# Optimization experiments

Measured on AMD Instinct MI355X. Metric: run time of the kernel, lower is better.

## Reference

```python
import jax, jax.numpy as jnp
import numpy as np
import math

H = 2048
NH = 16
HD = H // NH  # 128
EPS_LN = 1e-5
RES_SCALE_MAX = 0.3

def _nan_clean(x, lim=10000.0):
    return jnp.nan_to_num(x, nan=0.0, posinf=lim, neginf=-lim)

def setup_inputs() -> dict:
    key = jax.random.key(0)
    ks = jax.random.split(key, 12)
    B, S, T = 4, 2048, 256
    std = 1.0 / math.sqrt(H)
    return {
        "hidden_states": jax.random.normal(ks[0], (B, S, H), jnp.float32),
        "audio_tokens": jax.random.normal(ks[1], (B, T, H), jnp.float32),
        "attention_mask": jax.random.randint(ks[2], (B, T), 0, 2, jnp.int32),
        "Wq": jax.random.normal(ks[3], (H, H), jnp.float32) * std,
        "bq": jnp.zeros((H,), jnp.float32),
        "Wk": jax.random.normal(ks[4], (H, H), jnp.float32) * std,
        "bk": jnp.zeros((H,), jnp.float32),
        "Wv": jax.random.normal(ks[5], (H, H), jnp.float32) * std,
        "bv": jnp.zeros((H,), jnp.float32),
        "Wo": jax.random.normal(ks[6], (H, H), jnp.float32) * std,
        "bo": jnp.zeros((H,), jnp.float32),
        "ln_gamma": jnp.ones((H,), jnp.float32),
        "ln_beta": jnp.zeros((H,), jnp.float32),
        "residual_scale": jnp.float32(0.05),
    }

def reference(hidden_states, audio_tokens, attention_mask,
              Wq, bq, Wk, bk, Wv, bv, Wo, bo, ln_gamma, ln_beta, residual_scale):
    B, S, _ = hidden_states.shape
    T = audio_tokens.shape[1]
    hs = _nan_clean(hidden_states).astype(jnp.float32)
    at = _nan_clean(audio_tokens).astype(jnp.float32)
    # Q/K/V projections -> (B, heads, len, head_dim)
    def proj(x, W, b, L):
        y = x @ W.T + b
        return y.reshape(B, L, NH, HD).transpose(0, 2, 1, 3)
    q = _nan_clean(proj(hs, Wq, bq, S))
    k = _nan_clean(proj(at, Wk, bk, T))
    v = _nan_clean(proj(at, Wv, bv, T))
    scale = max(math.sqrt(HD), 1e-8)
    scores = jnp.einsum('bhsd,bhtd->bhst', q, k) / scale
    scores = jnp.clip(scores, -50.0, 50.0)
    scores = jnp.nan_to_num(scores, nan=0.0, posinf=50.0, neginf=-50.0)
    # mask: int 0/1 -> attend where > 0.5, broadcast (B,1,1,T)
    attend = (attention_mask.astype(jnp.float32) > 0.5)[:, None, None, :]
    scores = jnp.where(attend, scores, -10000.0)
    scores = jnp.clip(scores, -50.0, 50.0)
    probs = jax.nn.softmax(scores, axis=-1)
    probs = jnp.nan_to_num(probs, nan=0.0, posinf=1.0, neginf=0.0)
    probs = probs / (probs.sum(axis=-1, keepdims=True) + 1e-8)
    # dropout: eval mode -> identity
    ctx = jnp.einsum('bhst,bhtd->bhsd', probs, v)
    ctx = ctx.transpose(0, 2, 1, 3).reshape(B, S, H)
    delta = _nan_clean(ctx @ Wo.T + bo)
    rs = jnp.clip(residual_scale, 0.0, RES_SCALE_MAX)
    delta = rs * delta
    # LayerNorm (biased variance, like torch)
    mu = delta.mean(axis=-1, keepdims=True)
    var = jnp.mean((delta - mu) ** 2, axis=-1, keepdims=True)
    delta = (delta - mu) / jnp.sqrt(var + EPS_LN) * ln_gamma + ln_beta
    return delta
```

## Files before the change

kernel.cpp:

```cpp
#include <hip/hip_runtime.h>
#include <stdint.h>

typedef unsigned short u16;
typedef __attribute__((ext_vector_type(8))) __bf16 bf16x8;
typedef __attribute__((ext_vector_type(4))) float f32x4;

#define AS1 __attribute__((address_space(1)))
#define AS3 __attribute__((address_space(3)))

constexpr int HB = 4;
constexpr int SS = 2048;
constexpr int TT = 256;
constexpr int HH = 2048;
constexpr int NHEAD = 16;
constexpr int HD = 128;

__device__ __forceinline__ u16 f2b(float f) {
  union { float f; uint32_t u; } c; c.f = f;
  return (u16)((c.u + 0x7FFFu + ((c.u >> 16) & 1u)) >> 16);
}

__device__ __forceinline__ float b2f(uint32_t lo16) {
  union { uint32_t u; float f; } c; c.u = lo16 << 16;
  return c.f;
}

__global__ __launch_bounds__(256)
void cast_kernel(const float* __restrict__ in, u16* __restrict__ out, int n4) {
  int i = blockIdx.x * 256 + threadIdx.x;
  if (i >= n4) return;
  const float4 v = *(const float4*)(in + (size_t)i * 4);
  uint2 pk;
  pk.x = (uint32_t)f2b(v.x) | ((uint32_t)f2b(v.y) << 16);
  pk.y = (uint32_t)f2b(v.z) | ((uint32_t)f2b(v.w) << 16);
  *(uint2*)(out + (size_t)i * 4) = pk;
}

__global__ __launch_bounds__(256)
void cast_w_kernel(const float* __restrict__ w0, const float* __restrict__ w1,
                   const float* __restrict__ w2, const float* __restrict__ w3,
                   u16* __restrict__ o0, u16* __restrict__ o1,
                   u16* __restrict__ o2, u16* __restrict__ o3) {
  const float* src; u16* dst;
  switch (blockIdx.y) {
    case 0: src = w0; dst = o0; break;
    case 1: src = w1; dst = o1; break;
    case 2: src = w2; dst = o2; break;
    default: src = w3; dst = o3; break;
  }
  const int i = blockIdx.x * 256 + threadIdx.x;
  const float4 v = *(const float4*)(src + (size_t)i * 4);
  uint2 pk;
  pk.x = (uint32_t)f2b(v.x) | ((uint32_t)f2b(v.y) << 16);
  pk.y = (uint32_t)f2b(v.z) | ((uint32_t)f2b(v.w) << 16);
  *(uint2*)(dst + (size_t)i * 4) = pk;
}

template<int MODE>
__global__ __launch_bounds__(512, 2)
void gemm8(const u16* __restrict__ A, const u16* __restrict__ Bw,
           const float* __restrict__ bias, const float* __restrict__ rsp,
           void* __restrict__ outp) {
  constexpr int KD = 2048, NT = 64;
  constexpr int BUF = 16384;
  __shared__ u16 lds[3 * BUF];
  const int tid = threadIdx.x;
  const int wv = tid >> 6, ln = tid & 63;
  const int lq = ln >> 4, lr = ln & 15;
  const int wm = wv >> 2, wn = wv & 3;

  const int linb = blockIdx.y * 8 + blockIdx.x;
  const int ns = (linb & 7) * 32 + (linb >> 3);
  const int m0 = (ns >> 3) * 256;
  const int n0 = (ns & 7) * 256;

  int gOff[2];
#pragma unroll
  for (int c = 0; c < 2; ++c) {
    const int g = c * 512 + tid, sr = g >> 3, s = g & 7, l = s ^ (sr & 7);
    gOff[c] = (2 * sr + (l >> 2)) * KD + (l & 3) * 8;
  }
  const u16* Abase = A + (size_t)m0 * KD;
  const u16* Bbase = Bw + (size_t)n0 * KD;

  int aoff[8], boff[4];
#pragma unroll
  for (int m = 0; m < 8; ++m) {
    const int R = wm * 128 + m * 16 + lr, sr = R >> 1;
    aoff[m] = sr * 64 + ((((R & 1) << 2) + lq) ^ (sr & 7)) * 8;
  }
#pragma unroll
  for (int j = 0; j < 4; ++j) {
    const int R = wn * 64 + j * 16 + lr, sr = R >> 1;
    boff[j] = 8192 + sr * 64 + ((((R & 1) << 2) + lq) ^ (sr & 7)) * 8;
  }

#define STAGE_A(c, k0, buf)                                                      \
  __builtin_amdgcn_global_load_lds((AS1 const void*)(Abase + (k0) + gOff[c]),    \
      (AS3 void*)(lds + (buf) * BUF + ((c) * 512 + wv * 64) * 8), 16, 0, 0)
#define STAGE_B(c, k0, buf)                                                      \
  __builtin_amdgcn_global_load_lds((AS1 const void*)(Bbase + (k0) + gOff[c]),    \
      (AS3 void*)(lds + (buf) * BUF + 8192 + ((c) * 512 + wv * 64) * 8), 16, 0, 0)

  f32x4 acc[8][4];
#pragma unroll
  for (int i = 0; i < 8; ++i)
#pragma unroll
    for (int j = 0; j < 4; ++j) acc[i][j] = (f32x4){0.f, 0.f, 0.f, 0.f};

  STAGE_A(0, 0, 0); STAGE_A(1, 0, 0); STAGE_B(0, 0, 0); STAGE_B(1, 0, 0);
  STAGE_A(0, 32, 1); STAGE_A(1, 32, 1); STAGE_B(0, 32, 1); STAGE_B(1, 32, 1);
  asm volatile("s_waitcnt vmcnt(4)" ::: "memory");
  __builtin_amdgcn_s_barrier();

  int cur = 0;
  for (int t = 0; t < NT; ++t) {
    const u16* bb = lds + cur * BUF;
    const int stg = (cur >= 1) ? cur - 1 : 2;
    const int k2 = (t + 2) * 32;
    const bool doStage = (t + 2) < NT;
    bf16x8 af[4], bf[4];

#pragma unroll
    for (int j = 0; j < 4; ++j) bf[j] = *(const bf16x8*)(bb + boff[j]);
#pragma unroll
    for (int m = 0; m < 4; ++m) af[m] = *(const bf16x8*)(bb + aoff[m]);
    if (doStage) { STAGE_A(0, k2, stg); STAGE_A(1, k2, stg); }
    __builtin_amdgcn_s_barrier();
    asm volatile("s_waitcnt lgkmcnt(0)" ::: "memory");
    __builtin_amdgcn_sched_barrier(0);
    __builtin_amdgcn_s_setprio(1);
#pragma unroll
    for (int m = 0; m < 4; ++m)
#pragma unroll
      for (int j = 0; j < 4; ++j)
        acc[m][j] = __builtin_amdgcn_mfma_f32_16x16x32_bf16(af[m], bf[j], acc[m][j], 0, 0, 0);
    __builtin_amdgcn_s_setprio(0);
    __builtin_amdgcn_s_barrier();

#pragma unroll
    for (int m = 0; m < 4; ++m) af[m] = *(const bf16x8*)(bb + aoff[4 + m]);
    if (doStage) { STAGE_B(0, k2, stg); STAGE_B(1, k2, stg); }
    if (t < NT - 2)      asm volatile("s_waitcnt vmcnt(4)" ::: "memory");
    else if (t == NT - 2) asm volatile("s_waitcnt vmcnt(0)" ::: "memory");
    __builtin_amdgcn_s_barrier();
    asm volatile("s_waitcnt lgkmcnt(0)" ::: "memory");
    __builtin_amdgcn_sched_barrier(0);
    __builtin_amdgcn_s_setprio(1);
#pragma unroll
    for (int m = 0; m < 4; ++m)
#pragma unroll
      for (int j = 0; j < 4; ++j)
        acc[4 + m][j] = __builtin_amdgcn_mfma_f32_16x16x32_bf16(af[m], bf[j], acc[4 + m][j], 0, 0, 0);
    __builtin_amdgcn_s_setprio(0);
    __builtin_amdgcn_s_barrier();

    cur = (cur + 1 == 3) ? 0 : cur + 1;
  }
#undef STAGE_A
#undef STAGE_B

  float bj[4];
#pragma unroll
  for (int j = 0; j < 4; ++j) bj[j] = bias[n0 + wn * 64 + j * 16 + lr];
  float rsv = 0.f;
  if constexpr (MODE == 2 || MODE == 3) rsv = fminf(fmaxf(rsp[0], 0.0f), 0.3f);

#pragma unroll
  for (int i = 0; i < 8; ++i)
#pragma unroll
    for (int j = 0; j < 4; ++j)
#pragma unroll
      for (int r = 0; r < 4; ++r) {
        const int row = m0 + wm * 128 + i * 16 + lq * 4 + r;
        const int col = n0 + wn * 64 + j * 16 + lr;
        const float v = acc[i][j][r] + bj[j];
        if constexpr (MODE == 0) {
          ((u16*)outp)[(size_t)row * 2048 + col] = f2b(v);
        } else if constexpr (MODE == 2) {
          ((float*)outp)[(size_t)row * 2048 + col] = v * rsv;
        } else {
          ((u16*)outp)[(size_t)row * 2048 + col] = f2b(v * rsv);
        }
      }
}

__global__ __launch_bounds__(256, 2)
void gemm_kv(const u16* __restrict__ A, const u16* __restrict__ Wk,
             const u16* __restrict__ Wv, const float* __restrict__ bkp,
             const float* __restrict__ bvp, u16* __restrict__ Ko,
             u16* __restrict__ Vto) {
  constexpr int KD = 2048;
  __shared__ u16 sA[128 * 32];
  __shared__ u16 sB[128 * 32];
  const bool isV = blockIdx.z != 0;
  const u16* Bw = isV ? Wv : Wk;
  const float* bias = isV ? bvp : bkp;
  const int tid = threadIdx.x;
  const int wave = tid >> 6, lane = tid & 63;
  const int lq = lane >> 4, lr = lane & 15;
  const int wr = wave >> 1, wc = wave & 1;
  const int m0 = blockIdx.y * 128, n0 = blockIdx.x * 128;

  f32x4 acc[4][4];
#pragma unroll
  for (int i = 0; i < 4; ++i)
#pragma unroll
    for (int j = 0; j < 4; ++j) acc[i][j] = (f32x4){0.f, 0.f, 0.f, 0.f};

  for (int k0 = 0; k0 < KD; k0 += 32) {
#pragma unroll
    for (int it = 0; it < 2; ++it) {
      const int c = wave * 128 + it * 64 + lane;
      const int row = c >> 2, cc = c & 3;
      const u16* ga = A + (size_t)(m0 + row) * KD + (k0 + cc * 8);
      const u16* gb = Bw + (size_t)(n0 + row) * KD + (k0 + cc * 8);
      u16* la = sA + (size_t)(wave * 128 + it * 64) * 8;
      u16* lb = sB + (size_t)(wave * 128 + it * 64) * 8;
      __builtin_amdgcn_global_load_lds((AS1 const void*)ga, (AS3 void*)la, 16, 0, 0);
      __builtin_amdgcn_global_load_lds((AS1 const void*)gb, (AS3 void*)lb, 16, 0, 0);
    }
    asm volatile("s_waitcnt vmcnt(0)" ::: "memory");
    __syncthreads();

    bf16x8 af[4], bfr[4];
#pragma unroll
    for (int i = 0; i < 4; ++i)
      af[i] = *(const bf16x8*)(sA + (size_t)(wr * 64 + i * 16 + lr) * 32 + lq * 8);
#pragma unroll
    for (int j = 0; j < 4; ++j)
      bfr[j] = *(const bf16x8*)(sB + (size_t)(wc * 64 + j * 16 + lr) * 32 + lq * 8);
#pragma unroll
    for (int i = 0; i < 4; ++i)
#pragma unroll
      for (int j = 0; j < 4; ++j)
        acc[i][j] = __builtin_amdgcn_mfma_f32_16x16x32_bf16(af[i], bfr[j], acc[i][j], 0, 0, 0);
    __syncthreads();
  }

  float bj[4];
#pragma unroll
  for (int j = 0; j < 4; ++j) bj[j] = bias[n0 + wc * 64 + j * 16 + lr];

#pragma unroll
  for (int i = 0; i < 4; ++i)
#pragma unroll
    for (int j = 0; j < 4; ++j)
#pragma unroll
      for (int r = 0; r < 4; ++r) {
        const int row = m0 + wr * 64 + i * 16 + lq * 4 + r;
        const int col = n0 + wc * 64 + j * 16 + lr;
        const float v = acc[i][j][r] + bj[j];
        if (!isV) {
          Ko[(size_t)row * 2048 + col] = f2b(v);
        } else {
          Vto[(size_t)(row >> 8) * (2048 * 256) + (size_t)col * 256 + (row & 255)] = f2b(v);
        }
      }
}

__global__ __launch_bounds__(512, 2)
void attn_kernel(const u16* __restrict__ Q, const u16* __restrict__ Kb,
                 const u16* __restrict__ Vt, const int* __restrict__ mask,
                 u16* __restrict__ ctx) {
  __shared__ u16 sQ[128 * 128];
  __shared__ u16 sK[2][64 * 128];
  __shared__ u16 sVt[2][128 * 64];
  __shared__ u16 sP[8 * 16 * 72];

  const int tid = threadIdx.x;
  const int wv = tid >> 6, ln = tid & 63;
  const int lq = ln >> 4, lr = ln & 15;
  const int h = blockIdx.y, b = blockIdx.z;
  const int s0blk = blockIdx.x * 128;
  u16* sPw = sP + wv * (16 * 72);

  {
    const size_t qg = ((size_t)b * SS + s0blk) * HH + (size_t)h * HD;
#pragma unroll
    for (int it = 0; it < 4; ++it) {
      const int ub = it * 512 + wv * 64;
      const int u = ub + ln;
      const int row = u >> 4, slot = u & 15, src = slot ^ (row & 15);
      __builtin_amdgcn_global_load_lds((AS1 const void*)(Q + qg + (size_t)row * HH + src * 8),
                                       (AS3 void*)(sQ + (size_t)ub * 8), 16, 0, 0);
    }
  }
#define STAGE_KV(c)                                                                      \
  {                                                                                      \
    const int buf_ = (c) & 1;                                                            \
    _Pragma("unroll")                                                                    \
    for (int it = 0; it < 2; ++it) {                                                     \
      const int ub = it * 512 + wv * 64;                                                 \
      const int u = ub + ln;                                                             \
      const int row = u >> 4, slot = u & 15, src = slot ^ (row & 15);                    \
      const u16* g = Kb + ((size_t)b * TT + (c) * 64 + row) * HH + h * HD + src * 8;     \
      __builtin_amdgcn_global_load_lds((AS1 const void*)g,                               \
          (AS3 void*)(sK[buf_] + (size_t)ub * 8), 16, 0, 0);                             \
    }                                                                                    \
    _Pragma("unroll")                                                                    \
    for (int it = 0; it < 2; ++it) {                                                     \
      const int ub = it * 512 + wv * 64;                                                 \
      const int u = ub + ln;                                                             \
      const int row = u >> 3, slot = u & 7, src = slot ^ (row & 7);                      \
      const u16* g = Vt + ((size_t)b * HH + h * HD + row) * TT + (c) * 64 + src * 8;     \
      __builtin_amdgcn_global_load_lds((AS1 const void*)g,                               \
          (AS3 void*)(sVt[buf_] + (size_t)ub * 8), 16, 0, 0);                            \
    }                                                                                    \
  }
  STAGE_KV(0);
  STAGE_KV(1);

  const float scale = 0.08838834764831845f;
  float m[4] = {-INFINITY, -INFINITY, -INFINITY, -INFINITY};
  float l[4] = {0.f, 0.f, 0.f, 0.f};
  f32x4 o[8];
#pragma unroll
  for (int d0 = 0; d0 < 8; ++d0) o[d0] = (f32x4){0.f, 0.f, 0.f, 0.f};

  const int qrow = wv * 16 + lr;
  const int shsrc = ((lr >> 2) << 4) + lr;

  for (int c = 0; c < 4; ++c) {
    const int buf = c & 1;
    if (c < 3) asm volatile("s_waitcnt vmcnt(4)" ::: "memory");
    else       asm volatile("s_waitcnt vmcnt(0)" ::: "memory");
    __syncthreads();

    bf16x8 qf[4];
#pragma unroll
    for (int kd = 0; kd < 4; ++kd)
      qf[kd] = *(const bf16x8*)(sQ + (size_t)qrow * 128 + (size_t)((kd * 4 + lq) ^ lr) * 8);

    f32x4 sc[4];
#pragma unroll
    for (int tt = 0; tt < 4; ++tt) {
      f32x4 a = (f32x4){0.f, 0.f, 0.f, 0.f};
#pragma unroll
      for (int kd = 0; kd < 4; ++kd) {
        bf16x8 kf = *(const bf16x8*)(sK[buf] + (size_t)(tt * 16 + lr) * 128 + (size_t)((kd * 4 + lq) ^ lr) * 8);
        a = __builtin_amdgcn_mfma_f32_16x16x32_bf16(qf[kd], kf, a, 0, 0, 0);
      }
      sc[tt] = a;
    }

    float lm[4] = {-1e30f, -1e30f, -1e30f, -1e30f};
#pragma unroll
    for (int tt = 0; tt < 4; ++tt) {
      const int att = mask[b * TT + c * 64 + tt * 16 + lr];
#pragma unroll
      for (int r = 0; r < 4; ++r) {
        float v = sc[tt][r] * scale;
        v = fminf(fmaxf(v, -50.f), 50.f);
        v = att ? v : -50.f;
        sc[tt][r] = v;
        lm[r] = fmaxf(lm[r], v);
      }
    }
#pragma unroll
    for (int d = 1; d < 16; d <<= 1)
#pragma unroll
      for (int r = 0; r < 4; ++r) lm[r] = fmaxf(lm[r], __shfl_xor(lm[r], d));

    float alpha[4];
#pragma unroll
    for (int r = 0; r < 4; ++r) {
      const float mn = fmaxf(m[r], lm[r]);
      alpha[r] = __expf(m[r] - mn);
      m[r] = mn;
    }
    float ls[4] = {0.f, 0.f, 0.f, 0.f};
#pragma unroll
    for (int tt = 0; tt < 4; ++tt)
#pragma unroll
      for (int r = 0; r < 4; ++r) {
        const float p = __expf(sc[tt][r] - m[r]);
        sc[tt][r] = p;
        ls[r] += p;
      }
#pragma unroll
    for (int d = 1; d < 16; d <<= 1)
#pragma unroll
      for (int r = 0; r < 4; ++r) ls[r] += __shfl_xor(ls[r], d);
#pragma unroll
    for (int r = 0; r < 4; ++r) l[r] = l[r] * alpha[r] + ls[r];

    const float a0 = __shfl(alpha[0], shsrc), a1 = __shfl(alpha[1], shsrc);
    const float a2 = __shfl(alpha[2], shsrc), a3 = __shfl(alpha[3], shsrc);
    const int rsel = lr & 3;
    const float aq = rsel == 0 ? a0 : rsel == 1 ? a1 : rsel == 2 ? a2 : a3;
    if (!__all(aq >= 1.0f)) {
#pragma unroll
      for (int d0 = 0; d0 < 8; ++d0)
#pragma unroll
        for (int r = 0; r < 4; ++r) o[d0][r] *= aq;
    }

#pragma unroll
    for (int tt = 0; tt < 4; ++tt)
#pragma unroll
      for (int r = 0; r < 4; ++r)
        sPw[(size_t)(lq * 4 + r) * 72 + tt * 16 + lr] = f2b(sc[tt][r]);

    bf16x8 pf[2];
#pragma unroll
    for (int kt = 0; kt < 2; ++kt)
      pf[kt] = *(const bf16x8*)(sPw + (size_t)lr * 72 + kt * 32 + lq * 8);

#pragma unroll
    for (int d0 = 0; d0 < 8; ++d0)
#pragma unroll
      for (int kt = 0; kt < 2; ++kt) {
        bf16x8 vf = *(const bf16x8*)(sVt[buf] + (size_t)(d0 * 16 + lr) * 64 + (size_t)((kt * 4 + lq) ^ (lr & 7)) * 8);
        o[d0] = __builtin_amdgcn_mfma_f32_16x16x32_bf16(vf, pf[kt], o[d0], 0, 0, 0);
      }
    __syncthreads();
    if (c + 2 < 4) STAGE_KV(c + 2);
  }
#undef STAGE_KV

  const float i0 = __shfl(1.0f / l[0], shsrc), i1 = __shfl(1.0f / l[1], shsrc);
  const float i2 = __shfl(1.0f / l[2], shsrc), i3 = __shfl(1.0f / l[3], shsrc);
  const int rsel = lr & 3;
  const float iq = rsel == 0 ? i0 : rsel == 1 ? i1 : rsel == 2 ? i2 : i3;

  const size_t cbase = ((size_t)b * SS + s0blk + wv * 16 + lr) * HH + (size_t)h * HD;
#pragma unroll
  for (int d0 = 0; d0 < 8; ++d0) {
    uint2 w;
    w.x = (uint32_t)f2b(o[d0][0] * iq) | ((uint32_t)f2b(o[d0][1] * iq) << 16);
    w.y = (uint32_t)f2b(o[d0][2] * iq) | ((uint32_t)f2b(o[d0][3] * iq) << 16);
    *(uint2*)(ctx + cbase + d0 * 16 + lq * 4) = w;
  }
}

__global__ __launch_bounds__(256)
void ln_kernel(const u16* __restrict__ in, float* __restrict__ out,
               const float* __restrict__ gamma, const float* __restrict__ beta) {
  const int row = blockIdx.x, tid = threadIdx.x;
  const u16* x = in + (size_t)row * 2048;
  const uint4 raw = *(const uint4*)(x + tid * 8);
  float xv[8];
  xv[0] = b2f(raw.x & 0xFFFFu); xv[1] = b2f(raw.x >> 16);
  xv[2] = b2f(raw.y & 0xFFFFu); xv[3] = b2f(raw.y >> 16);
  xv[4] = b2f(raw.z & 0xFFFFu); xv[5] = b2f(raw.z >> 16);
  xv[6] = b2f(raw.w & 0xFFFFu); xv[7] = b2f(raw.w >> 16);
  float s = 0.f, ss = 0.f;
#pragma unroll
  for (int i = 0; i < 8; ++i) { s += xv[i]; ss += xv[i] * xv[i]; }
#pragma unroll
  for (int d = 1; d < 64; d <<= 1) {
    s += __shfl_xor(s, d);
    ss += __shfl_xor(ss, d);
  }
  __shared__ float rbuf[8];
  const int w = tid >> 6;
  if ((tid & 63) == 0) { rbuf[w] = s; rbuf[4 + w] = ss; }
  __syncthreads();
  s = rbuf[0] + rbuf[1] + rbuf[2] + rbuf[3];
  ss = rbuf[4] + rbuf[5] + rbuf[6] + rbuf[7];
  const float mu = s * (1.0f / 2048.0f);
  const float var = ss * (1.0f / 2048.0f) - mu * mu;
  const float inv = rsqrtf(var + 1e-5f);
  const float4 g0 = *(const float4*)(gamma + tid * 8);
  const float4 g1 = *(const float4*)(gamma + tid * 8 + 4);
  const float4 b0 = *(const float4*)(beta + tid * 8);
  const float4 b1 = *(const float4*)(beta + tid * 8 + 4);
  float4 y0, y1;
  y0.x = (xv[0] - mu) * inv * g0.x + b0.x;
  y0.y = (xv[1] - mu) * inv * g0.y + b0.y;
  y0.z = (xv[2] - mu) * inv * g0.z + b0.z;
  y0.w = (xv[3] - mu) * inv * g0.w + b0.w;
  y1.x = (xv[4] - mu) * inv * g1.x + b1.x;
  y1.y = (xv[5] - mu) * inv * g1.y + b1.y;
  y1.z = (xv[6] - mu) * inv * g1.z + b1.z;
  y1.w = (xv[7] - mu) * inv * g1.w + b1.w;
  float* o = out + (size_t)row * 2048 + tid * 8;
  *(float4*)o = y0;
  *(float4*)(o + 4) = y1;
}

extern "C" void kernel_launch(void* const* d_in, const int* in_sizes, int n_in,
                              void* d_out, int out_size, void* d_ws, size_t ws_size,
                              hipStream_t stream) {
  (void)in_sizes; (void)n_in; (void)out_size; (void)ws_size;
  const float* hs = (const float*)d_in[0];
  const float* at = (const float*)d_in[1];
  const int* mask = (const int*)d_in[2];
  const float* Wq = (const float*)d_in[3];
  const float* bq = (const float*)d_in[4];
  const float* Wk = (const float*)d_in[5];
  const float* bk = (const float*)d_in[6];
  const float* Wv = (const float*)d_in[7];
  const float* bv = (const float*)d_in[8];
  const float* Wo = (const float*)d_in[9];
  const float* bo = (const float*)d_in[10];
  const float* lg = (const float*)d_in[11];
  const float* lb = (const float*)d_in[12];
  const float* rs = (const float*)d_in[13];

  u16* hs_bf = (u16*)d_ws;
  u16* at_bf = hs_bf + 16777216;
  u16* Wq_bf = at_bf + 2097152;
  u16* Wk_bf = Wq_bf + 4194304;
  u16* Wv_bf = Wk_bf + 4194304;
  u16* Wo_bf = Wv_bf + 4194304;
  u16* Q_bf  = Wo_bf + 4194304;
  u16* K_bf  = Q_bf + 16777216;
  u16* Vt_bf = K_bf + 2097152;
  u16* ctx_bf = hs_bf;
  u16* delta_bf = Q_bf;

  cast_kernel<<<16384, 256, 0, stream>>>(hs, hs_bf, 4194304);
  cast_kernel<<<2048, 256, 0, stream>>>(at, at_bf, 524288);
  cast_w_kernel<<<dim3(4096, 4), 256, 0, stream>>>(Wq, Wk, Wv, Wo,
                                                   Wq_bf, Wk_bf, Wv_bf, Wo_bf);

  gemm8<0><<<dim3(8, 32), 512, 0, stream>>>(hs_bf, Wq_bf, bq, nullptr, Q_bf);
  gemm_kv<<<dim3(16, 8, 2), 256, 0, stream>>>(at_bf, Wk_bf, Wv_bf, bk, bv, K_bf, Vt_bf);

  attn_kernel<<<dim3(16, 16, 4), 512, 0, stream>>>(Q_bf, K_bf, Vt_bf, mask, ctx_bf);

  gemm8<3><<<dim3(8, 32), 512, 0, stream>>>(ctx_bf, Wo_bf, bo, rs, delta_bf);
  ln_kernel<<<8192, 256, 0, stream>>>(delta_bf, (float*)d_out, lg, lb);
}
```

Baseline: 295.1 us.

## Deepen GEMM pipelines to four LDS stages and fuse cast kernels

The Q/O projection GEMM moves from three to four LDS stages, preloads the next K-step's fragments into registers, and uses one barrier per iteration instead of three. The K/V GEMM replaces its synchronous single-buffer loop with a swizzled four-stage asynchronous global-to-LDS pipeline. The three fp32-to-bf16 cast launches are merged into one kernel. The larger LDS footprint of the main GEMM (128 KB) likely allows only one block per CU despite the launch bound requesting two.

```diff
diff --git a/kernel.cpp b/kernel.cpp
--- a/kernel.cpp
+++ b/kernel.cpp
@@ -26,34 +26,26 @@
 }
 
 __global__ __launch_bounds__(256)
-void cast_kernel(const float* __restrict__ in, u16* __restrict__ out, int n4) {
-  int i = blockIdx.x * 256 + threadIdx.x;
-  if (i >= n4) return;
-  const float4 v = *(const float4*)(in + (size_t)i * 4);
+void cast_all(const float* __restrict__ hs, const float* __restrict__ at,
+              const float* __restrict__ wq, const float* __restrict__ wk,
+              const float* __restrict__ wv, const float* __restrict__ wo,
+              u16* __restrict__ o_hs, u16* __restrict__ o_at,
+              u16* __restrict__ o_wq, u16* __restrict__ o_wk,
+              u16* __restrict__ o_wv, u16* __restrict__ o_wo) {
+  const int b = blockIdx.x;
+  const float* src; u16* dst; int base;
+  if (b < 16384)      { src = hs; dst = o_hs; base = 0; }
+  else if (b < 18432) { src = at; dst = o_at; base = 16384; }
+  else if (b < 22528) { src = wq; dst = o_wq; base = 18432; }
+  else if (b < 26624) { src = wk; dst = o_wk; base = 22528; }
+  else if (b < 30720) { src = wv; dst = o_wv; base = 26624; }
+  else                { src = wo; dst = o_wo; base = 30720; }
+  const size_t i = (size_t)(b - base) * 256 + threadIdx.x;
+  const float4 v = *(const float4*)(src + i * 4);
   uint2 pk;
   pk.x = (uint32_t)f2b(v.x) | ((uint32_t)f2b(v.y) << 16);
   pk.y = (uint32_t)f2b(v.z) | ((uint32_t)f2b(v.w) << 16);
-  *(uint2*)(out + (size_t)i * 4) = pk;
-}
-
-__global__ __launch_bounds__(256)
-void cast_w_kernel(const float* __restrict__ w0, const float* __restrict__ w1,
-                   const float* __restrict__ w2, const float* __restrict__ w3,
-                   u16* __restrict__ o0, u16* __restrict__ o1,
-                   u16* __restrict__ o2, u16* __restrict__ o3) {
-  const float* src; u16* dst;
-  switch (blockIdx.y) {
-    case 0: src = w0; dst = o0; break;
-    case 1: src = w1; dst = o1; break;
-    case 2: src = w2; dst = o2; break;
-    default: src = w3; dst = o3; break;
-  }
-  const int i = blockIdx.x * 256 + threadIdx.x;
-  const float4 v = *(const float4*)(src + (size_t)i * 4);
-  uint2 pk;
-  pk.x = (uint32_t)f2b(v.x) | ((uint32_t)f2b(v.y) << 16);
-  pk.y = (uint32_t)f2b(v.z) | ((uint32_t)f2b(v.w) << 16);
-  *(uint2*)(dst + (size_t)i * 4) = pk;
+  *(uint2*)(dst + i * 4) = pk;
 }
 
 template<int MODE>
@@ -63,7 +55,7 @@
            void* __restrict__ outp) {
   constexpr int KD = 2048, NT = 64;
   constexpr int BUF = 16384;
-  __shared__ u16 lds[3 * BUF];
+  __shared__ u16 lds[4 * BUF];
   const int tid = threadIdx.x;
   const int wv = tid >> 6, ln = tid & 63;
   const int lq = ln >> 4, lr = ln & 15;
@@ -108,26 +100,31 @@
 #pragma unroll
     for (int j = 0; j < 4; ++j) acc[i][j] = (f32x4){0.f, 0.f, 0.f, 0.f};
 
-  STAGE_A(0, 0, 0); STAGE_A(1, 0, 0); STAGE_B(0, 0, 0); STAGE_B(1, 0, 0);
+  STAGE_A(0, 0, 0);  STAGE_A(1, 0, 0);  STAGE_B(0, 0, 0);  STAGE_B(1, 0, 0);
   STAGE_A(0, 32, 1); STAGE_A(1, 32, 1); STAGE_B(0, 32, 1); STAGE_B(1, 32, 1);
-  asm volatile("s_waitcnt vmcnt(4)" ::: "memory");
+  STAGE_A(0, 64, 2); STAGE_A(1, 64, 2); STAGE_B(0, 64, 2); STAGE_B(1, 64, 2);
+  asm volatile("s_waitcnt vmcnt(8)" ::: "memory");
   __builtin_amdgcn_s_barrier();
-
-  int cur = 0;
+  __builtin_amdgcn_sched_barrier(0);
+
+  bf16x8 af[4], bf[4], afn[4];
+#pragma unroll
+  for (int j = 0; j < 4; ++j) bf[j] = *(const bf16x8*)(lds + boff[j]);
+#pragma unroll
+  for (int m = 0; m < 4; ++m) af[m] = *(const bf16x8*)(lds + aoff[m]);
+  __builtin_amdgcn_sched_barrier(0);
+
   for (int t = 0; t < NT; ++t) {
-    const u16* bb = lds + cur * BUF;
-    const int stg = (cur >= 1) ? cur - 1 : 2;
-    const int k2 = (t + 2) * 32;
-    const bool doStage = (t + 2) < NT;
-    bf16x8 af[4], bf[4];
-
-#pragma unroll
-    for (int j = 0; j < 4; ++j) bf[j] = *(const bf16x8*)(bb + boff[j]);
-#pragma unroll
-    for (int m = 0; m < 4; ++m) af[m] = *(const bf16x8*)(bb + aoff[m]);
-    if (doStage) { STAGE_A(0, k2, stg); STAGE_A(1, k2, stg); }
-    __builtin_amdgcn_s_barrier();
-    asm volatile("s_waitcnt lgkmcnt(0)" ::: "memory");
+    const u16* bb = lds + (t & 3) * BUF;
+    const u16* bn = lds + ((t + 1) & 3) * BUF;
+    const int stg = (t + 3) & 3;
+    const int k3 = (t + 3) * 32;
+    const bool doStage = (t + 3) < NT;
+
+#pragma unroll
+    for (int m = 0; m < 4; ++m) afn[m] = *(const bf16x8*)(bb + aoff[4 + m]);
+    if (doStage) { STAGE_A(0, k3, stg); STAGE_A(1, k3, stg); }
+    asm volatile("s_waitcnt lgkmcnt(4)" ::: "memory");
     __builtin_amdgcn_sched_barrier(0);
     __builtin_amdgcn_s_setprio(1);
 #pragma unroll
@@ -136,26 +133,29 @@
       for (int j = 0; j < 4; ++j)
         acc[m][j] = __builtin_amdgcn_mfma_f32_16x16x32_bf16(af[m], bf[j], acc[m][j], 0, 0, 0);
     __builtin_amdgcn_s_setprio(0);
+    if (doStage) { STAGE_B(0, k3, stg); STAGE_B(1, k3, stg); }
+    if (t < NT - 3)       asm volatile("s_waitcnt vmcnt(8)" ::: "memory");
+    else if (t == NT - 3) asm volatile("s_waitcnt vmcnt(4)" ::: "memory");
+    else                  asm volatile("s_waitcnt vmcnt(0)" ::: "memory");
+    asm volatile("s_waitcnt lgkmcnt(0)" ::: "memory");
     __builtin_amdgcn_s_barrier();
-
-#pragma unroll
-    for (int m = 0; m < 4; ++m) af[m] = *(const bf16x8*)(bb + aoff[4 + m]);
-    if (doStage) { STAGE_B(0, k2, stg); STAGE_B(1, k2, stg); }
-    if (t < NT - 2)      asm volatile("s_waitcnt vmcnt(4)" ::: "memory");
-    else if (t == NT - 2) asm volatile("s_waitcnt vmcnt(0)" ::: "memory");
-    __builtin_amdgcn_s_barrier();
-    asm volatile("s_waitcnt lgkmcnt(0)" ::: "memory");
     __builtin_amdgcn_sched_barrier(0);
+    if (t + 1 < NT) {
+#pragma unroll
+      for (int m = 0; m < 4; ++m) af[m] = *(const bf16x8*)(bn + aoff[m]);
+    }
     __builtin_amdgcn_s_setprio(1);
 #pragma unroll
     for (int m = 0; m < 4; ++m)
 #pragma unroll
       for (int j = 0; j < 4; ++j)
-        acc[4 + m][j] = __builtin_amdgcn_mfma_f32_16x16x32_bf16(af[m], bf[j], acc[4 + m][j], 0, 0, 0);
+        acc[4 + m][j] = __builtin_amdgcn_mfma_f32_16x16x32_bf16(afn[m], bf[j], acc[4 + m][j], 0, 0, 0);
     __builtin_amdgcn_s_setprio(0);
-    __builtin_amdgcn_s_barrier();
-
-    cur = (cur + 1 == 3) ? 0 : cur + 1;
+    if (t + 1 < NT) {
+#pragma unroll
+      for (int j = 0; j < 4; ++j) bf[j] = *(const bf16x8*)(bn + boff[j]);
+    }
+    __builtin_amdgcn_sched_barrier(0);
   }
 #undef STAGE_A
 #undef STAGE_B
@@ -190,9 +190,9 @@
              const u16* __restrict__ Wv, const float* __restrict__ bkp,
              const float* __restrict__ bvp, u16* __restrict__ Ko,
              u16* __restrict__ Vto) {
-  constexpr int KD = 2048;
-  __shared__ u16 sA[128 * 32];
-  __shared__ u16 sB[128 * 32];
+  constexpr int KD = 2048, NT = 64;
+  constexpr int BUFE = 8192;
+  __shared__ u16 lds[4 * BUFE];
   const bool isV = blockIdx.z != 0;
   const u16* Bw = isV ? Wv : Wk;
   const float* bias = isV ? bvp : bkp;
@@ -202,41 +202,85 @@
   const int wr = wave >> 1, wc = wave & 1;
   const int m0 = blockIdx.y * 128, n0 = blockIdx.x * 128;
 
+  int gOff[2];
+#pragma unroll
+  for (int c = 0; c < 2; ++c) {
+    const int g = c * 256 + tid, sr = g >> 3, s = g & 7, l = s ^ (sr & 7);
+    gOff[c] = (2 * sr + (l >> 2)) * KD + (l & 3) * 8;
+  }
+  const u16* Abase = A + (size_t)m0 * KD;
+  const u16* Bbase = Bw + (size_t)n0 * KD;
+
+  int aoff[4], boff[4];
+#pragma unroll
+  for (int i = 0; i < 4; ++i) {
+    const int R = wr * 64 + i * 16 + lr, sr = R >> 1;
+    aoff[i] = sr * 64 + ((((R & 1) << 2) + lq) ^ (sr & 7)) * 8;
+  }
+#pragma unroll
+  for (int j = 0; j < 4; ++j) {
+    const int R = wc * 64 + j * 16 + lr, sr = R >> 1;
+    boff[j] = 4096 + sr * 64 + ((((R & 1) << 2) + lq) ^ (sr & 7)) * 8;
+  }
+
+#define KV_STAGE(t3, buf)                                                         \
+  {                                                                               \
+    _Pragma("unroll")                                                             \
+    for (int c_ = 0; c_ < 2; ++c_) {                                              \
+      __builtin_amdgcn_global_load_lds(                                           \
+          (AS1 const void*)(Abase + (t3) * 32 + gOff[c_]),                        \
+          (AS3 void*)(lds + (buf) * BUFE + (c_ * 256 + wave * 64) * 8), 16, 0, 0);\
+      __builtin_amdgcn_global_load_lds(                                           \
+          (AS1 const void*)(Bbase + (t3) * 32 + gOff[c_]),                        \
+          (AS3 void*)(lds + (buf) * BUFE + 4096 + (c_ * 256 + wave * 64) * 8),    \
+          16, 0, 0);                                                              \
+    }                                                                             \
+  }
+
   f32x4 acc[4][4];
 #pragma unroll
   for (int i = 0; i < 4; ++i)
 #pragma unroll
     for (int j = 0; j < 4; ++j) acc[i][j] = (f32x4){0.f, 0.f, 0.f, 0.f};
 
-  for (int k0 = 0; k0 < KD; k0 += 32) {
-#pragma unroll
-    for (int it = 0; it < 2; ++it) {
-      const int c = wave * 128 + it * 64 + lane;
-      const int row = c >> 2, cc = c & 3;
-      const u16* ga = A + (size_t)(m0 + row) * KD + (k0 + cc * 8);
-      const u16* gb = Bw + (size_t)(n0 + row) * KD + (k0 + cc * 8);
-      u16* la = sA + (size_t)(wave * 128 + it * 64) * 8;
-      u16* lb = sB + (size_t)(wave * 128 + it * 64) * 8;
-      __builtin_amdgcn_global_load_lds((AS1 const void*)ga, (AS3 void*)la, 16, 0, 0);
-      __builtin_amdgcn_global_load_lds((AS1 const void*)gb, (AS3 void*)lb, 16, 0, 0);
-    }
-    asm volatile("s_waitcnt vmcnt(0)" ::: "memory");
-    __syncthreads();
-
-    bf16x8 af[4], bfr[4];
-#pragma unroll
-    for (int i = 0; i < 4; ++i)
-      af[i] = *(const bf16x8*)(sA + (size_t)(wr * 64 + i * 16 + lr) * 32 + lq * 8);
-#pragma unroll
-    for (int j = 0; j < 4; ++j)
-      bfr[j] = *(const bf16x8*)(sB + (size_t)(wc * 64 + j * 16 + lr) * 32 + lq * 8);
+  KV_STAGE(0, 0); KV_STAGE(1, 1); KV_STAGE(2, 2);
+  asm volatile("s_waitcnt vmcnt(8)" ::: "memory");
+  __builtin_amdgcn_s_barrier();
+  __builtin_amdgcn_sched_barrier(0);
+
+  bf16x8 af[4], bfr[4];
+#pragma unroll
+  for (int i = 0; i < 4; ++i) af[i] = *(const bf16x8*)(lds + aoff[i]);
+#pragma unroll
+  for (int j = 0; j < 4; ++j) bfr[j] = *(const bf16x8*)(lds + boff[j]);
+  __builtin_amdgcn_sched_barrier(0);
+
+  for (int t = 0; t < NT; ++t) {
+    if (t + 3 < NT) KV_STAGE(t + 3, (t + 3) & 3);
+    asm volatile("s_waitcnt lgkmcnt(0)" ::: "memory");
+    __builtin_amdgcn_sched_barrier(0);
+    __builtin_amdgcn_s_setprio(1);
 #pragma unroll
     for (int i = 0; i < 4; ++i)
 #pragma unroll
       for (int j = 0; j < 4; ++j)
         acc[i][j] = __builtin_amdgcn_mfma_f32_16x16x32_bf16(af[i], bfr[j], acc[i][j], 0, 0, 0);
-    __syncthreads();
-  }
+    __builtin_amdgcn_s_setprio(0);
+    if (t < NT - 3)       asm volatile("s_waitcnt vmcnt(8)" ::: "memory");
+    else if (t == NT - 3) asm volatile("s_waitcnt vmcnt(4)" ::: "memory");
+    else                  asm volatile("s_waitcnt vmcnt(0)" ::: "memory");
+    __builtin_amdgcn_s_barrier();
+    __builtin_amdgcn_sched_barrier(0);
+    if (t + 1 < NT) {
+      const u16* bn = lds + ((t + 1) & 3) * BUFE;
+#pragma unroll
+      for (int i = 0; i < 4; ++i) af[i] = *(const bf16x8*)(bn + aoff[i]);
+#pragma unroll
+      for (int j = 0; j < 4; ++j) bfr[j] = *(const bf16x8*)(bn + boff[j]);
+    }
+    __builtin_amdgcn_sched_barrier(0);
+  }
+#undef KV_STAGE
 
   float bj[4];
 #pragma unroll
@@ -511,10 +555,8 @@
   u16* ctx_bf = hs_bf;
   u16* delta_bf = Q_bf;
 
-  cast_kernel<<<16384, 256, 0, stream>>>(hs, hs_bf, 4194304);
-  cast_kernel<<<2048, 256, 0, stream>>>(at, at_bf, 524288);
-  cast_w_kernel<<<dim3(4096, 4), 256, 0, stream>>>(Wq, Wk, Wv, Wo,
-                                                   Wq_bf, Wk_bf, Wv_bf, Wo_bf);
+  cast_all<<<34816, 256, 0, stream>>>(hs, at, Wq, Wk, Wv, Wo,
+                                      hs_bf, at_bf, Wq_bf, Wk_bf, Wv_bf, Wo_bf);
 
   gemm8<0><<<dim3(8, 32), 512, 0, stream>>>(hs_bf, Wq_bf, bq, nullptr, Q_bf);
   gemm_kv<<<dim3(16, 8, 2), 256, 0, stream>>>(at_bf, Wk_bf, Wv_bf, bk, bv, K_bf, Vt_bf);
```

Measured after the change: 266.7 us. 1.11x faster.
